# Performance work log

Hardware: AMD Instinct MI355X
Metric: run time of the kernel (lower is better)

## Reference

```python
import jax, jax.numpy as jnp
import numpy as np

ITERS = 3; S = 8; I = 64; E = 64; C = 64; DIN = 128; SLOT = 128; H = 256
B = 64; N = 4096; EPS = 1e-8

def _ln(x, g, b):
    m = jnp.mean(x, -1, keepdims=True)
    v = jnp.var(x, -1, keepdims=True)
    return (x - m) * jax.lax.rsqrt(v + 1e-5) * g + b

def _gru(x, h, Wih, Whh, bih, bhh):
    # torch nn.GRUCell math; W stored as [in, 3*hidden]
    gi = x @ Wih + bih
    gh = h @ Whh + bhh
    ir, iz, inn = jnp.split(gi, 3, -1)
    hr, hz, hn = jnp.split(gh, 3, -1)
    r = jax.nn.sigmoid(ir + hr)
    z = jax.nn.sigmoid(iz + hz)
    n = jnp.tanh(inn + r * hn)
    return (1.0 - z) * n + z * h

def setup_inputs() -> dict:
    k = jax.random.split(jax.random.key(0), 32)
    d = {}
    d['slots_bck'] = jax.random.normal(k[0], (B, 1, SLOT), jnp.float32)
    d['inputs'] = jax.random.normal(k[1], (B, N, DIN), jnp.float32)
    d['protos'] = jax.random.normal(k[2], (C, I), jnp.float32)
    d['ext_noise'] = jax.random.normal(k[3], (B, S, E), jnp.float32)
    d['int_noise'] = jax.random.normal(k[4], (B, S, C), jnp.float32)
    u = jax.random.uniform(k[5], (ITERS, B, S, C), jnp.float32, 1e-6, 1.0 - 1e-6)
    d['gumbel'] = -jnp.log(-jnp.log(u))
    d['tau'] = 1
    w = lambda i, shape, s=0.05: jax.random.normal(k[i], shape, jnp.float32) * s
    d['ext_mu'] = w(6, (1, 1, E)); d['ext_log_sigma'] = w(7, (1, 1, E))
    d['int_mu'] = w(8, (1, 1, C)); d['int_log_sigma'] = w(9, (1, 1, C))
    d['ln_in_g'] = jnp.ones((DIN,)); d['ln_in_b'] = jnp.zeros((DIN,))
    d['ln_p_g'] = jnp.ones((I,)); d['ln_p_b'] = jnp.zeros((I,))
    d['ln_mi_g'] = jnp.ones((I,)); d['ln_mi_b'] = jnp.zeros((I,))
    d['ln_me_g'] = jnp.ones((E,)); d['ln_me_b'] = jnp.zeros((E,))
    d['Wq'] = w(10, (SLOT, SLOT)); d['Wk'] = w(11, (DIN, SLOT))
    d['Wv'] = w(12, (DIN, SLOT)); d['Wp'] = w(13, (I, I))
    d['gi_Wih'] = w(14, (I, 3 * I)); d['gi_Whh'] = w(15, (I, 3 * I))
    d['gi_bih'] = jnp.zeros((3 * I,)); d['gi_bhh'] = jnp.zeros((3 * I,))
    d['ge_Wih'] = w(16, (E, 3 * E)); d['ge_Whh'] = w(17, (E, 3 * E))
    d['ge_bih'] = jnp.zeros((3 * E,)); d['ge_bhh'] = jnp.zeros((3 * E,))
    d['mi_W1'] = w(18, (I, H)); d['mi_b1'] = jnp.zeros((H,))
    d['mi_W2'] = w(19, (H, I)); d['mi_b2'] = jnp.zeros((I,))
    d['me_W1'] = w(20, (E, H)); d['me_b1'] = jnp.zeros((H,))
    d['me_W2'] = w(21, (H, E)); d['me_b2'] = jnp.zeros((E,))
    return d

def reference(slots_bck, inputs, protos, ext_noise, int_noise, gumbel,
              ext_mu, ext_log_sigma, int_mu, int_log_sigma,
              ln_in_g, ln_in_b, ln_p_g, ln_p_b, ln_mi_g, ln_mi_b, ln_me_g, ln_me_b,
              Wq, Wk, Wv, Wp,
              gi_Wih, gi_Whh, gi_bih, gi_bhh, ge_Wih, ge_Whh, ge_bih, ge_bhh,
              mi_W1, mi_b1, mi_W2, mi_b2, me_W1, me_b1, me_W2, me_b2, tau):
    Bsz = inputs.shape[0]
    slots_ext = ext_mu + jnp.exp(ext_log_sigma) * ext_noise            # [B,S,E]
    logits_pi = int_mu + jnp.exp(int_log_sigma) * int_noise            # [B,S,C]
    x = _ln(inputs, ln_in_g, ln_in_b)
    kk = (x @ Wk) * (SLOT ** -0.5)                                     # [B,N,SLOT]
    vv = x @ Wv                                                        # [B,N,SLOT]
    p = _ln(protos, ln_p_g, ln_p_b) @ Wp                               # [C,I]
    attn_vis = None
    for i in range(ITERS):
        pi = jax.nn.softmax((logits_pi + gumbel[i]) / tau, axis=-1)    # soft gumbel-softmax
        slots_int = pi @ p                                             # [B,S,I]
        slots_obj = jnp.concatenate([slots_int, slots_ext], -1)        # [B,S,SLOT]
        slots = jnp.concatenate([slots_bck, slots_obj[:, 1:]], 1)
        q = slots @ Wq                                                 # [B,S,SLOT]
        attn_logits = jnp.einsum('bnd,bsd->bns', kk, q)
        attn_vis = jax.nn.softmax(attn_logits, -1)                     # softmax over slots
        attn = attn_vis + EPS
        attn = attn / jnp.sum(attn, -2, keepdims=True)                 # renorm over inputs
        updates = jnp.einsum('bns,bnd->bsd', attn, vv)                 # [B,S,SLOT]
        upd_int, upd_ext = updates[..., :I], updates[..., I:]
        slots_ext = _gru(upd_ext.reshape(-1, E), slots_ext.reshape(-1, E),
                         ge_Wih, ge_Whh, ge_bih, ge_bhh).reshape(Bsz, S, E)
        if i < ITERS - 1:
            h = _ln(slots_ext, ln_me_g, ln_me_b)
            slots_ext = slots_ext + (jax.nn.relu(h @ me_W1 + me_b1) @ me_W2 + me_b2)
        int_upd = _gru(upd_int.reshape(-1, I), slots_int.reshape(-1, I),
                       gi_Wih, gi_Whh, gi_bih, gi_bhh).reshape(Bsz, S, I)
        if i < ITERS - 1:
            h = _ln(int_upd, ln_mi_g, ln_mi_b)
            int_upd = int_upd + (jax.nn.relu(h @ mi_W1 + mi_b1) @ mi_W2 + mi_b2)
        logits_pi = (int_upd @ p.T) * (I ** -0.5)
    return slots_ext[:, 1:], logits_pi[:, 1:], attn_vis
```

## Files before the change

kernel.cpp:

```cpp
#include <hip/hip_runtime.h>
#include <hip/hip_bf16.h>
#include <stdint.h>

typedef unsigned short u16;
#define DEVFN static __device__ __forceinline__

typedef __attribute__((ext_vector_type(8))) short bf16x8;
typedef __attribute__((ext_vector_type(4))) float f32x4;

constexpr int   kB   = 64;
constexpr int   kN   = 4096;
constexpr float kEPS = 1e-8f;
constexpr float kLNE = 1e-5f;
constexpr float kKSC = 0.08838834764831845f;
constexpr float kISC = 0.125f;

DEVFN u16 f2bf(float f) {
    union { float f; uint32_t u; } x; x.f = f;
    uint32_t r = (x.u + 0x7fffu + ((x.u >> 16) & 1u)) >> 16;
    return (u16)r;
}
DEVFN uint32_t pk2(float lo, float hi) {
    __hip_bfloat162 h = __float22bfloat162_rn(make_float2(lo, hi));
    uint32_t u; __builtin_memcpy(&u, &h, 4); return u;
}
DEVFN u16 bf1(float f) {
    __hip_bfloat16 h = __float2bfloat16(f);
    u16 u; __builtin_memcpy(&u, &h, 2); return u;
}
DEVFN float sigf(float x) { return 1.0f / (1.0f + __expf(-x)); }

__global__ void kinit(const float* __restrict__ ext_mu, const float* __restrict__ ext_ls,
                      const float* __restrict__ int_mu, const float* __restrict__ int_ls,
                      const float* __restrict__ ext_noise, const float* __restrict__ int_noise,
                      float* __restrict__ sext, float* __restrict__ lpi)
{
    int t = blockIdx.x * 256 + threadIdx.x;
    int e = t & 63;
    sext[t] = ext_mu[e] + __expf(ext_ls[e]) * ext_noise[t];
    lpi[t]  = int_mu[e] + __expf(int_ls[e]) * int_noise[t];
}

__global__ void kwprep(const float* __restrict__ Wk, const float* __restrict__ Wv,
                       u16* __restrict__ WT)
{
    int idx = blockIdx.x * 256 + threadIdx.x;
    int k = idx >> 8, c = idx & 255;
    float v = (c < 128) ? Wk[k * 128 + c] * kKSC : Wv[k * 128 + (c - 128)];
    WT[(size_t)c * 128 + k] = f2bf(v);
}

__global__ void kprep(const float* __restrict__ protos, const float* __restrict__ Wp,
                      const float* __restrict__ lpg, const float* __restrict__ lpb,
                      float* __restrict__ p, float* __restrict__ pT)
{
    __shared__ float pl[64][65];
    __shared__ float mS[64], sS[64];
    int t = threadIdx.x;
    for (int idx = t; idx < 64 * 64; idx += 256) pl[idx >> 6][idx & 63] = protos[idx];
    __syncthreads();
    if (t < 64) {
        float sm = 0.f, sq = 0.f;
        for (int k = 0; k < 64; ++k) { float v = pl[t][k]; sm += v; sq += v * v; }
        float m = sm * (1.0f / 64.0f);
        float var = sq * (1.0f / 64.0f) - m * m;
        mS[t] = m; sS[t] = rsqrtf(var + kLNE);
    }
    __syncthreads();
    for (int idx = t; idx < 64 * 64; idx += 256) {
        int r = idx >> 6, c = idx & 63;
        pl[r][c] = (pl[r][c] - mS[r]) * sS[r] * lpg[c] + lpb[c];
    }
    __syncthreads();
    for (int idx = t; idx < 64 * 64; idx += 256) {
        int r = idx >> 6, c = idx & 63;
        float acc = 0.f;
        for (int k = 0; k < 64; ++k) acc += pl[r][k] * Wp[k * 64 + c];
        p[r * 64 + c] = acc;
        pT[c * 64 + r] = acc;
    }
}

__global__ __launch_bounds__(256) void kmain(const float* __restrict__ inputs,
                                             const u16* __restrict__ WT,
                                             const float* __restrict__ lng, const float* __restrict__ lnb,
                                             u16* __restrict__ kk, u16* __restrict__ vvT,
                                             float* __restrict__ vpart)
{
    __shared__ u16 At[64 * 128];
    const int t = threadIdx.x;
    const int blk = blockIdx.x;
    const int b = blk >> 6;
    const int n0 = (blk & 63) * 64;
    const float* inp = inputs + ((size_t)(b * kN + n0)) * 128;

    const int row = t >> 2, q4 = t & 3;
    float4 xv[8];
    #pragma unroll
    for (int j = 0; j < 8; ++j) xv[j] = ((const float4*)inp)[row * 32 + q4 * 8 + j];

    float sm = 0.f, sq = 0.f;
    #pragma unroll
    for (int j = 0; j < 8; ++j) {
        sm += xv[j].x + xv[j].y + xv[j].z + xv[j].w;
        sq += xv[j].x * xv[j].x + xv[j].y * xv[j].y + xv[j].z * xv[j].z + xv[j].w * xv[j].w;
    }
    sm += __shfl_xor(sm, 1); sm += __shfl_xor(sm, 2);
    sq += __shfl_xor(sq, 1); sq += __shfl_xor(sq, 2);
    const float mn  = sm * (1.0f / 128.0f);
    const float var = sq * (1.0f / 128.0f) - mn * mn;
    const float sc  = rsqrtf(var + kLNE);

    const float4* g4p = ((const float4*)lng) + q4 * 8;
    const float4* b4p = ((const float4*)lnb) + q4 * 8;
    #pragma unroll
    for (int jj = 0; jj < 4; ++jj) {
        const float4 a0 = xv[jj * 2], a1 = xv[jj * 2 + 1];
        const float4 g0 = g4p[jj * 2], g1 = g4p[jj * 2 + 1];
        const float4 c0 = b4p[jj * 2], c1 = b4p[jj * 2 + 1];
        uint4 pk;
        pk.x = pk2((a0.x - mn) * sc * g0.x + c0.x, (a0.y - mn) * sc * g0.y + c0.y);
        pk.y = pk2((a0.z - mn) * sc * g0.z + c0.z, (a0.w - mn) * sc * g0.w + c0.w);
        pk.z = pk2((a1.x - mn) * sc * g1.x + c1.x, (a1.y - mn) * sc * g1.y + c1.y);
        pk.w = pk2((a1.z - mn) * sc * g1.z + c1.z, (a1.w - mn) * sc * g1.w + c1.w);
        const int chunk = (q4 * 4 + jj) ^ (row & 7);
        *(uint4*)((char*)At + row * 256 + chunk * 16) = pk;
    }
    __syncthreads();

    const int w  = t >> 6;
    const int l  = t & 63;
    const int lg = l >> 4;
    const int lr = l & 15;
    const bool iskk = (w < 2);

    f32x4 acc[4][4];
    #pragma unroll
    for (int i = 0; i < 4; ++i)
        #pragma unroll
        for (int j = 0; j < 4; ++j) acc[i][j] = (f32x4){0.f, 0.f, 0.f, 0.f};

    #pragma unroll
    for (int ks = 0; ks < 4; ++ks) {
        bf16x8 wf[4], xf[4];
        #pragma unroll
        for (int i = 0; i < 4; ++i)
            wf[i] = *(const bf16x8*)(WT + (size_t)(w * 64 + 16 * i + lr) * 128 + ks * 32 + lg * 8);
        #pragma unroll
        for (int i = 0; i < 4; ++i) {
            const int r2 = 16 * i + lr;
            const int chunk = (ks * 4 + lg) ^ (r2 & 7);
            xf[i] = *(const bf16x8*)((const char*)At + r2 * 256 + chunk * 16);
        }
        if (iskk) {
            #pragma unroll
            for (int i = 0; i < 4; ++i)
                #pragma unroll
                for (int j = 0; j < 4; ++j)
                    acc[i][j] = __builtin_amdgcn_mfma_f32_16x16x32_bf16(wf[i], xf[j], acc[i][j], 0, 0, 0);
        } else {
            #pragma unroll
            for (int i = 0; i < 4; ++i)
                #pragma unroll
                for (int j = 0; j < 4; ++j)
                    acc[i][j] = __builtin_amdgcn_mfma_f32_16x16x32_bf16(xf[i], wf[j], acc[i][j], 0, 0, 0);
        }
    }

    if (iskk) {
        #pragma unroll
        for (int nn = 0; nn < 4; ++nn) {
            const size_t rb = ((size_t)(b * kN) + n0 + 16 * nn + lr) * 128;
            #pragma unroll
            for (int cm = 0; cm < 4; ++cm) {
                uint2 pk;
                pk.x = pk2(acc[cm][nn][0], acc[cm][nn][1]);
                pk.y = pk2(acc[cm][nn][2], acc[cm][nn][3]);
                *(uint2*)(kk + rb + w * 64 + 16 * cm + lg * 4) = pk;
            }
        }
    } else {
        #pragma unroll
        for (int ct = 0; ct < 4; ++ct) {
            const int d = (w - 2) * 64 + 16 * ct + lr;
            const size_t db = ((size_t)b * 128 + d) * (size_t)kN;
            #pragma unroll
            for (int m = 0; m < 4; ++m) {
                uint2 pk;
                pk.x = pk2(acc[m][ct][0], acc[m][ct][1]);
                pk.y = pk2(acc[m][ct][2], acc[m][ct][3]);
                *(uint2*)(vvT + db + n0 + 16 * m + lg * 4) = pk;
            }
            float sv = 0.f;
            #pragma unroll
            for (int m = 0; m < 4; ++m)
                #pragma unroll
                for (int r = 0; r < 4; ++r) sv += acc[m][ct][r];
            sv += __shfl_xor(sv, 16);
            sv += __shfl_xor(sv, 32);
            if (lg == 0) vpart[(size_t)blk * 128 + d] = sv;
        }
    }
}

__global__ void kvvsum(const float* __restrict__ part, float* __restrict__ vvsum)
{
    int t = blockIdx.x * 256 + threadIdx.x;
    int b = t >> 7, c = t & 127;
    float s = 0.f;
    const float* pp = part + (size_t)b * 64 * 128 + c;
    for (int nb = 0; nb < 64; ++nb) s += pp[nb * 128];
    vvsum[t] = s;
}

__global__ void kslots(const float* __restrict__ lpi, const float* __restrict__ gum,
                       const void* __restrict__ taup,
                       const float* __restrict__ p,
                       const float* __restrict__ sbck, const float* __restrict__ sext,
                       const float* __restrict__ Wq,
                       float* __restrict__ sint, float* __restrict__ q)
{
    __shared__ float piL[64];
    __shared__ float sv[128];
    const int bs = blockIdx.x;
    const int b = bs >> 3, s = bs & 7;
    const int t = threadIdx.x;
    float inv_tau = 1.0f;
    {
        int iv = *(const int*)taup;
        if (iv > 0 && iv < 1000000) inv_tau = 1.0f / (float)iv;
        else {
            float fv = *(const float*)taup;
            if (fv > 1e-6f && fv < 1e6f) inv_tau = 1.0f / fv;
        }
    }
    if (t < 64) {
        float l = (lpi[bs * 64 + t] + gum[bs * 64 + t]) * inv_tau;
        float m = l;
        #pragma unroll
        for (int d = 32; d >= 1; d >>= 1) m = fmaxf(m, __shfl_xor(m, d));
        float e = __expf(l - m);
        float smv = e;
        #pragma unroll
        for (int d = 32; d >= 1; d >>= 1) smv += __shfl_xor(smv, d);
        piL[t] = e / smv;
    }
    __syncthreads();
    if (t < 64) {
        float acc = 0.f;
        for (int c = 0; c < 64; ++c) acc += piL[c] * p[c * 64 + t];
        sint[bs * 64 + t] = acc;
        if (s == 0) {
            sv[t]      = sbck[b * 128 + t];
            sv[64 + t] = sbck[b * 128 + 64 + t];
        } else {
            sv[t]      = acc;
            sv[64 + t] = sext[bs * 64 + t];
        }
    }
    __syncthreads();
    {
        float acc = 0.f;
        for (int k = 0; k < 128; ++k) acc += sv[k] * Wq[k * 128 + t];
        q[bs * 128 + t] = acc;
    }
}

__global__ __launch_bounds__(256) void kattn(const u16* __restrict__ kk, const u16* __restrict__ vvT,
                                             const float* __restrict__ q,
                                             float* __restrict__ attn_out,
                                             float* __restrict__ pu, float* __restrict__ pcs,
                                             const int wvis)
{
    __shared__ u16 qbf[16][128];
    __shared__ u16 aB[4][16][40];
    __shared__ float pwU[4][8][132];
    __shared__ float csL[4][8];
    const int t = threadIdx.x;
    const int blk = blockIdx.x;
    const int b = blk >> 3;
    const int nb = blk & 7;
    const int w = t >> 6, l = t & 63, lg = l >> 4, lr = l & 15;

    {
        float4 v = ((const float4*)(q + (size_t)b * 1024))[t];
        uint2 pk;
        pk.x = pk2(v.x, v.y);
        pk.y = pk2(v.z, v.w);
        *(uint2*)&qbf[t >> 5][(t & 31) * 4] = pk;
        ((uint32_t*)qbf)[512 + t] = 0u;
        ((uint32_t*)qbf)[768 + (t & 255)] = 0u;
    }
    __syncthreads();

    bf16x8 qf[4];
    #pragma unroll
    for (int ks = 0; ks < 4; ++ks) qf[ks] = *(const bf16x8*)&qbf[lr][ks * 32 + lg * 8];

    f32x4 apv[8];
    #pragma unroll
    for (int dt = 0; dt < 8; ++dt) apv[dt] = (f32x4){0.f, 0.f, 0.f, 0.f};
    float cs0 = 0.f, cs1 = 0.f, cs2 = 0.f, cs3 = 0.f;

    const size_t kkb = (size_t)(b * kN) * 128;
    const size_t vvb = (size_t)b * 128 * (size_t)kN;

    for (int ch = 0; ch < 4; ++ch) {
        const int nbase = nb * 512 + w * 128 + ch * 32;
        #pragma unroll
        for (int c2 = 0; c2 < 2; ++c2) {
            const int n16 = nbase + 16 * c2;
            f32x4 pl = (f32x4){0.f, 0.f, 0.f, 0.f};
            #pragma unroll
            for (int ks = 0; ks < 4; ++ks) {
                bf16x8 bfr = *(const bf16x8*)(kk + kkb + (size_t)(n16 + lr) * 128 + ks * 32 + lg * 8);
                pl = __builtin_amdgcn_mfma_f32_16x16x32_bf16(qf[ks], bfr, pl, 0, 0, 0);
            }
            float m = fmaxf(fmaxf(pl[0], pl[1]), fmaxf(pl[2], pl[3]));
            m = fmaxf(m, __shfl_xor(m, 16));
            float e0 = __expf(pl[0] - m), e1 = __expf(pl[1] - m);
            float e2 = __expf(pl[2] - m), e3 = __expf(pl[3] - m);
            float smv = e0 + e1 + e2 + e3;
            smv += __shfl_xor(smv, 16);
            const float inv = 1.0f / smv;
            const float a0 = e0 * inv, a1 = e1 * inv, a2 = e2 * inv, a3 = e3 * inv;
            if (lg < 2) {
                cs0 += a0; cs1 += a1; cs2 += a2; cs3 += a3;
                if (wvis)
                    *(float4*)(attn_out + ((size_t)(b * kN) + n16 + lr) * 8 + lg * 4) =
                        make_float4(a0, a1, a2, a3);
                const int s0 = lg * 4, nn = 16 * c2 + lr;
                aB[w][s0 + 0][nn] = bf1(a0);
                aB[w][s0 + 1][nn] = bf1(a1);
                aB[w][s0 + 2][nn] = bf1(a2);
                aB[w][s0 + 3][nn] = bf1(a3);
            }
        }
        bf16x8 af = *(const bf16x8*)&aB[w][lr][lg * 8];
        #pragma unroll
        for (int dt = 0; dt < 8; ++dt) {
            bf16x8 vfr = *(const bf16x8*)(vvT + vvb + (size_t)(16 * dt + lr) * kN + nbase + lg * 8);
            apv[dt] = __builtin_amdgcn_mfma_f32_16x16x32_bf16(vfr, af, apv[dt], 0, 0, 0);
        }
    }

    if (lr < 8) {
        #pragma unroll
        for (int dt = 0; dt < 8; ++dt)
            *(float4*)&pwU[w][lr][16 * dt + lg * 4] =
                make_float4(apv[dt][0], apv[dt][1], apv[dt][2], apv[dt][3]);
    }
    #pragma unroll
    for (int d = 8; d >= 1; d >>= 1) {
        cs0 += __shfl_xor(cs0, d); cs1 += __shfl_xor(cs1, d);
        cs2 += __shfl_xor(cs2, d); cs3 += __shfl_xor(cs3, d);
    }
    if (lr == 0 && lg < 2) {
        csL[w][lg * 4 + 0] = cs0; csL[w][lg * 4 + 1] = cs1;
        csL[w][lg * 4 + 2] = cs2; csL[w][lg * 4 + 3] = cs3;
    }
    __syncthreads();
    {
        const int s = t >> 5, dq = t & 31;
        float4 r0 = *(const float4*)&pwU[0][s][dq * 4];
        float4 r1 = *(const float4*)&pwU[1][s][dq * 4];
        float4 r2 = *(const float4*)&pwU[2][s][dq * 4];
        float4 r3 = *(const float4*)&pwU[3][s][dq * 4];
        float4 o;
        o.x = r0.x + r1.x + r2.x + r3.x;
        o.y = r0.y + r1.y + r2.y + r3.y;
        o.z = r0.z + r1.z + r2.z + r3.z;
        o.w = r0.w + r1.w + r2.w + r3.w;
        *(float4*)(pu + (size_t)blk * 1024 + s * 128 + dq * 4) = o;
    }
    if (t < 8) pcs[blk * 8 + t] = csL[0][t] + csL[1][t] + csL[2][t] + csL[3][t];
}

__global__ __launch_bounds__(256) void kupdate(
    const float* __restrict__ pu, const float* __restrict__ pcs,
    const float* __restrict__ vvsum, const float* __restrict__ sint,
    float* __restrict__ sext, float* __restrict__ lpi,
    const float* __restrict__ giWih, const float* __restrict__ giWhh,
    const float* __restrict__ gibih, const float* __restrict__ gibhh,
    const float* __restrict__ geWih, const float* __restrict__ geWhh,
    const float* __restrict__ gebih, const float* __restrict__ gebhh,
    const float* __restrict__ miW1, const float* __restrict__ mib1,
    const float* __restrict__ miW2, const float* __restrict__ mib2,
    const float* __restrict__ meW1, const float* __restrict__ meb1,
    const float* __restrict__ meW2, const float* __restrict__ meb2,
    const float* __restrict__ lmig, const float* __restrict__ lmib,
    const float* __restrict__ lmeg, const float* __restrict__ lmeb,
    const float* __restrict__ pT, float* __restrict__ out, const int last)
{
    __shared__ float uL[128], hA[64], hB[64];
    __shared__ float g1[192], g2[192];
    __shared__ float tmp[256];
    __shared__ float outE[64], outI[64];
    const int bs = blockIdx.x;
    const int b = bs >> 3, s = bs & 7;
    const int t = threadIdx.x;

    if (t < 128) {
        float num = 0.f;
        for (int nb = 0; nb < 8; ++nb) num += pu[((size_t)(b * 8 + nb)) * 1024 + s * 128 + t];
        float den = 4096.0f * kEPS;
        for (int nb = 0; nb < 8; ++nb) den += pcs[(b * 8 + nb) * 8 + s];
        uL[t] = (num + kEPS * vvsum[b * 128 + t]) / den;
    } else if (t < 192) {
        hA[t - 128] = sext[bs * 64 + (t - 128)];
    } else {
        hB[t - 192] = sint[bs * 64 + (t - 192)];
    }
    __syncthreads();
    if (t < 192) {
        float a = gebih[t], bb = gebhh[t];
        for (int k = 0; k < 64; ++k) {
            a  = fmaf(uL[64 + k], geWih[k * 192 + t], a);
            bb = fmaf(hA[k],      geWhh[k * 192 + t], bb);
        }
        g1[t] = a; g2[t] = bb;
    }
    __syncthreads();
    if (t < 64) {
        float r = sigf(g1[t] + g2[t]);
        float z = sigf(g1[64 + t] + g2[64 + t]);
        float nn = tanhf(g1[128 + t] + r * g2[128 + t]);
        outE[t] = (1.0f - z) * nn + z * hA[t];
    }
    __syncthreads();
    if (t < 192) {
        float a = gibih[t], bb = gibhh[t];
        for (int k = 0; k < 64; ++k) {
            a  = fmaf(uL[k], giWih[k * 192 + t], a);
            bb = fmaf(hB[k], giWhh[k * 192 + t], bb);
        }
        g1[t] = a; g2[t] = bb;
    }
    __syncthreads();
    if (t < 64) {
        float r = sigf(g1[t] + g2[t]);
        float z = sigf(g1[64 + t] + g2[64 + t]);
        float nn = tanhf(g1[128 + t] + r * g2[128 + t]);
        outI[t] = (1.0f - z) * nn + z * hB[t];
    }
    __syncthreads();
    if (!last) {
        if (t < 64) {
            float v = outE[t];
            float sm = v, sq = v * v;
            #pragma unroll
            for (int d = 32; d >= 1; d >>= 1) { sm += __shfl_xor(sm, d); sq += __shfl_xor(sq, d); }
            float m = sm * (1.0f / 64.0f), var = sq * (1.0f / 64.0f) - m * m;
            g1[t] = (v - m) * rsqrtf(var + kLNE) * lmeg[t] + lmeb[t];
        }
        __syncthreads();
        {
            float a = meb1[t];
            for (int k = 0; k < 64; ++k) a = fmaf(g1[k], meW1[k * 256 + t], a);
            tmp[t] = fmaxf(a, 0.0f);
        }
        __syncthreads();
        if (t < 64) {
            float o = meb2[t];
            for (int j = 0; j < 256; ++j) o = fmaf(tmp[j], meW2[j * 64 + t], o);
            outE[t] += o;
        }
        __syncthreads();
        if (t < 64) {
            float v = outI[t];
            float sm = v, sq = v * v;
            #pragma unroll
            for (int d = 32; d >= 1; d >>= 1) { sm += __shfl_xor(sm, d); sq += __shfl_xor(sq, d); }
            float m = sm * (1.0f / 64.0f), var = sq * (1.0f / 64.0f) - m * m;
            g1[t] = (v - m) * rsqrtf(var + kLNE) * lmig[t] + lmib[t];
        }
        __syncthreads();
        {
            float a = mib1[t];
            for (int k = 0; k < 64; ++k) a = fmaf(g1[k], miW1[k * 256 + t], a);
            tmp[t] = fmaxf(a, 0.0f);
        }
        __syncthreads();
        if (t < 64) {
            float o = mib2[t];
            for (int j = 0; j < 256; ++j) o = fmaf(tmp[j], miW2[j * 64 + t], o);
            outI[t] += o;
        }
        __syncthreads();
    }
    if (t < 64) {
        float lg = 0.f;
        for (int k = 0; k < 64; ++k) lg = fmaf(outI[k], pT[k * 64 + t], lg);
        lg *= kISC;
        lpi[bs * 64 + t] = lg;
        if (last && s > 0) out[28672 + (b * 7 + (s - 1)) * 64 + t] = lg;
    } else if (t < 128) {
        int c = t - 64;
        float v = outE[c];
        sext[bs * 64 + c] = v;
        if (last && s > 0) out[(b * 7 + (s - 1)) * 64 + c] = v;
    }
}

extern "C" void kernel_launch(void* const* d_in, const int* in_sizes, int n_in,
                              void* d_out, int out_size, void* d_ws, size_t ws_size,
                              hipStream_t stream)
{
    (void)in_sizes; (void)n_in; (void)out_size; (void)ws_size;
    const float* slots_bck = (const float*)d_in[0];
    const float* inputs    = (const float*)d_in[1];
    const float* protos    = (const float*)d_in[2];
    const float* ext_noise = (const float*)d_in[3];
    const float* int_noise = (const float*)d_in[4];
    const float* gumbel    = (const float*)d_in[5];
    const void*  taup      = d_in[6];
    const float* ext_mu    = (const float*)d_in[7];
    const float* ext_ls    = (const float*)d_in[8];
    const float* int_mu    = (const float*)d_in[9];
    const float* int_ls    = (const float*)d_in[10];
    const float* ln_in_g   = (const float*)d_in[11];
    const float* ln_in_b   = (const float*)d_in[12];
    const float* ln_p_g    = (const float*)d_in[13];
    const float* ln_p_b    = (const float*)d_in[14];
    const float* ln_mi_g   = (const float*)d_in[15];
    const float* ln_mi_b   = (const float*)d_in[16];
    const float* ln_me_g   = (const float*)d_in[17];
    const float* ln_me_b   = (const float*)d_in[18];
    const float* Wq        = (const float*)d_in[19];
    const float* Wk        = (const float*)d_in[20];
    const float* Wv        = (const float*)d_in[21];
    const float* Wp        = (const float*)d_in[22];
    const float* giWih     = (const float*)d_in[23];
    const float* giWhh     = (const float*)d_in[24];
    const float* gibih     = (const float*)d_in[25];
    const float* gibhh     = (const float*)d_in[26];
    const float* geWih     = (const float*)d_in[27];
    const float* geWhh     = (const float*)d_in[28];
    const float* gebih     = (const float*)d_in[29];
    const float* gebhh     = (const float*)d_in[30];
    const float* miW1      = (const float*)d_in[31];
    const float* mib1      = (const float*)d_in[32];
    const float* miW2      = (const float*)d_in[33];
    const float* mib2      = (const float*)d_in[34];
    const float* meW1      = (const float*)d_in[35];
    const float* meb1      = (const float*)d_in[36];
    const float* meW2      = (const float*)d_in[37];
    const float* meb2      = (const float*)d_in[38];
    float* out = (float*)d_out;

    char* ws = (char*)d_ws;
    size_t o = 0;
    auto alloc = [&](size_t bytes) { size_t r = o; o += (bytes + 255) & ~(size_t)255; return r; };
    u16*   kkp   = (u16*)  (ws + alloc((size_t)kB * kN * 128 * 2));
    u16*   vvTp  = (u16*)  (ws + alloc((size_t)kB * kN * 128 * 2));
    u16*   WT    = (u16*)  (ws + alloc(256 * 128 * 2));
    float* vpart = (float*)(ws + alloc((size_t)4096 * 128 * 4));
    float* vvsum = (float*)(ws + alloc(8192 * 4));
    float* pbuf  = (float*)(ws + alloc(4096 * 4));
    float* pT    = (float*)(ws + alloc(4096 * 4));
    float* sext  = (float*)(ws + alloc(32768 * 4));
    float* lpi   = (float*)(ws + alloc(32768 * 4));
    float* sint  = (float*)(ws + alloc(32768 * 4));
    float* q     = (float*)(ws + alloc(65536 * 4));
    float* pu    = (float*)(ws + alloc((size_t)512 * 1024 * 4));
    float* pcs   = (float*)(ws + alloc(512 * 8 * 4));

    kinit<<<128, 256, 0, stream>>>(ext_mu, ext_ls, int_mu, int_ls, ext_noise, int_noise, sext, lpi);
    kwprep<<<128, 256, 0, stream>>>(Wk, Wv, WT);
    kprep<<<1, 256, 0, stream>>>(protos, Wp, ln_p_g, ln_p_b, pbuf, pT);
    kmain<<<4096, 256, 0, stream>>>(inputs, WT, ln_in_g, ln_in_b, kkp, vvTp, vpart);
    kvvsum<<<32, 256, 0, stream>>>(vpart, vvsum);

    for (int i = 0; i < 3; ++i) {
        kslots<<<512, 128, 0, stream>>>(lpi, gumbel + (size_t)i * 32768, taup, pbuf,
                                        slots_bck, sext, Wq, sint, q);
        kattn<<<512, 256, 0, stream>>>(kkp, vvTp, q, out + 57344, pu, pcs, (i == 2) ? 1 : 0);
        kupdate<<<512, 256, 0, stream>>>(pu, pcs, vvsum, sint, sext, lpi,
                                         giWih, giWhh, gibih, gibhh,
                                         geWih, geWhh, gebih, gebhh,
                                         miW1, mib1, miW2, mib2,
                                         meW1, meb1, meW2, meb2,
                                         ln_mi_g, ln_mi_b, ln_me_g, ln_me_b,
                                         pT, out, (i == 2) ? 1 : 0);
    }
}
```

Before: 318.0 us.

## Fuse setup kernels, fold slot/query computation into update kernel, coalesce LN loads

Merges the init, weight-transpose and prototype prep kernels into one launch, folds the vv-sum reduction into the first slots launch, and moves the per-iteration slot sampling and query projection into the tail of the update kernel, so the loop runs two launches per iteration instead of three. The input layernorm in the main kernel now loads with a fully coalesced float4 pattern and reduces across 32 lanes with shuffles. The aim is to cut launch overhead and improve load coalescing. The cost is more shuffle work per row and a longer update kernel.

```diff
diff --git a/kernel.cpp b/kernel.cpp
--- a/kernel.cpp
+++ b/kernel.cpp
@@ -29,34 +29,45 @@
     u16 u; __builtin_memcpy(&u, &h, 2); return u;
 }
 DEVFN float sigf(float x) { return 1.0f / (1.0f + __expf(-x)); }
-
-__global__ void kinit(const float* __restrict__ ext_mu, const float* __restrict__ ext_ls,
-                      const float* __restrict__ int_mu, const float* __restrict__ int_ls,
-                      const float* __restrict__ ext_noise, const float* __restrict__ int_noise,
-                      float* __restrict__ sext, float* __restrict__ lpi)
-{
-    int t = blockIdx.x * 256 + threadIdx.x;
-    int e = t & 63;
-    sext[t] = ext_mu[e] + __expf(ext_ls[e]) * ext_noise[t];
-    lpi[t]  = int_mu[e] + __expf(int_ls[e]) * int_noise[t];
-}
-
-__global__ void kwprep(const float* __restrict__ Wk, const float* __restrict__ Wv,
-                       u16* __restrict__ WT)
-{
-    int idx = blockIdx.x * 256 + threadIdx.x;
-    int k = idx >> 8, c = idx & 255;
-    float v = (c < 128) ? Wk[k * 128 + c] * kKSC : Wv[k * 128 + (c - 128)];
-    WT[(size_t)c * 128 + k] = f2bf(v);
-}
-
-__global__ void kprep(const float* __restrict__ protos, const float* __restrict__ Wp,
-                      const float* __restrict__ lpg, const float* __restrict__ lpb,
-                      float* __restrict__ p, float* __restrict__ pT)
+DEVFN float read_tau(const void* taup) {
+    float inv_tau = 1.0f;
+    int iv = *(const int*)taup;
+    if (iv > 0 && iv < 1000000) inv_tau = 1.0f / (float)iv;
+    else {
+        float fv = *(const float*)taup;
+        if (fv > 1e-6f && fv < 1e6f) inv_tau = 1.0f / fv;
+    }
+    return inv_tau;
+}
+
+__global__ void ksetup(const float* __restrict__ ext_mu, const float* __restrict__ ext_ls,
+                       const float* __restrict__ int_mu, const float* __restrict__ int_ls,
+                       const float* __restrict__ ext_noise, const float* __restrict__ int_noise,
+                       float* __restrict__ sext, float* __restrict__ lpi,
+                       const float* __restrict__ Wk, const float* __restrict__ Wv,
+                       u16* __restrict__ WT,
+                       const float* __restrict__ protos, const float* __restrict__ Wp,
+                       const float* __restrict__ lpg, const float* __restrict__ lpb,
+                       float* __restrict__ p, float* __restrict__ pT)
 {
     __shared__ float pl[64][65];
     __shared__ float mS[64], sS[64];
-    int t = threadIdx.x;
+    const int blk = blockIdx.x;
+    const int t = threadIdx.x;
+    if (blk < 128) {
+        int idx = blk * 256 + t;
+        int e = idx & 63;
+        sext[idx] = ext_mu[e] + __expf(ext_ls[e]) * ext_noise[idx];
+        lpi[idx]  = int_mu[e] + __expf(int_ls[e]) * int_noise[idx];
+        return;
+    }
+    if (blk < 256) {
+        int idx = (blk - 128) * 256 + t;
+        int k = idx >> 8, c = idx & 255;
+        float v = (c < 128) ? Wk[k * 128 + c] * kKSC : Wv[k * 128 + (c - 128)];
+        WT[(size_t)c * 128 + k] = f2bf(v);
+        return;
+    }
     for (int idx = t; idx < 64 * 64; idx += 256) pl[idx >> 6][idx & 63] = protos[idx];
     __syncthreads();
     if (t < 64) {
@@ -94,37 +105,37 @@
     const int n0 = (blk & 63) * 64;
     const float* inp = inputs + ((size_t)(b * kN + n0)) * 128;
 
-    const int row = t >> 2, q4 = t & 3;
     float4 xv[8];
     #pragma unroll
-    for (int j = 0; j < 8; ++j) xv[j] = ((const float4*)inp)[row * 32 + q4 * 8 + j];
-
-    float sm = 0.f, sq = 0.f;
+    for (int j = 0; j < 8; ++j) xv[j] = ((const float4*)inp)[t + j * 256];
+
+    float s[8], qq[8];
     #pragma unroll
     for (int j = 0; j < 8; ++j) {
-        sm += xv[j].x + xv[j].y + xv[j].z + xv[j].w;
-        sq += xv[j].x * xv[j].x + xv[j].y * xv[j].y + xv[j].z * xv[j].z + xv[j].w * xv[j].w;
-    }
-    sm += __shfl_xor(sm, 1); sm += __shfl_xor(sm, 2);
-    sq += __shfl_xor(sq, 1); sq += __shfl_xor(sq, 2);
-    const float mn  = sm * (1.0f / 128.0f);
-    const float var = sq * (1.0f / 128.0f) - mn * mn;
-    const float sc  = rsqrtf(var + kLNE);
-
-    const float4* g4p = ((const float4*)lng) + q4 * 8;
-    const float4* b4p = ((const float4*)lnb) + q4 * 8;
-    #pragma unroll
-    for (int jj = 0; jj < 4; ++jj) {
-        const float4 a0 = xv[jj * 2], a1 = xv[jj * 2 + 1];
-        const float4 g0 = g4p[jj * 2], g1 = g4p[jj * 2 + 1];
-        const float4 c0 = b4p[jj * 2], c1 = b4p[jj * 2 + 1];
-        uint4 pk;
-        pk.x = pk2((a0.x - mn) * sc * g0.x + c0.x, (a0.y - mn) * sc * g0.y + c0.y);
-        pk.y = pk2((a0.z - mn) * sc * g0.z + c0.z, (a0.w - mn) * sc * g0.w + c0.w);
-        pk.z = pk2((a1.x - mn) * sc * g1.x + c1.x, (a1.y - mn) * sc * g1.y + c1.y);
-        pk.w = pk2((a1.z - mn) * sc * g1.z + c1.z, (a1.w - mn) * sc * g1.w + c1.w);
-        const int chunk = (q4 * 4 + jj) ^ (row & 7);
-        *(uint4*)((char*)At + row * 256 + chunk * 16) = pk;
+        s[j]  = xv[j].x + xv[j].y + xv[j].z + xv[j].w;
+        qq[j] = xv[j].x * xv[j].x + xv[j].y * xv[j].y + xv[j].z * xv[j].z + xv[j].w * xv[j].w;
+    }
+    #pragma unroll
+    for (int d = 16; d >= 1; d >>= 1) {
+        #pragma unroll
+        for (int j = 0; j < 8; ++j) {
+            s[j]  += __shfl_xor(s[j], d);
+            qq[j] += __shfl_xor(qq[j], d);
+        }
+    }
+    const int col4 = t & 31;
+    const float4 g4 = ((const float4*)lng)[col4];
+    const float4 b4 = ((const float4*)lnb)[col4];
+    #pragma unroll
+    for (int j = 0; j < 8; ++j) {
+        const int row = (t >> 5) + 8 * j;
+        const float m   = s[j] * (1.0f / 128.0f);
+        const float var = qq[j] * (1.0f / 128.0f) - m * m;
+        const float sc  = rsqrtf(var + kLNE);
+        uint32_t p0 = pk2((xv[j].x - m) * sc * g4.x + b4.x, (xv[j].y - m) * sc * g4.y + b4.y);
+        uint32_t p1 = pk2((xv[j].z - m) * sc * g4.z + b4.z, (xv[j].w - m) * sc * g4.w + b4.w);
+        const int byteoff = row * 256 + (((col4 >> 1) ^ (row & 7)) << 4) + ((col4 & 1) << 3);
+        *(uint2*)((char*)At + byteoff) = make_uint2(p0, p1);
     }
     __syncthreads();
 
@@ -203,37 +214,29 @@
     }
 }
 
-__global__ void kvvsum(const float* __restrict__ part, float* __restrict__ vvsum)
-{
-    int t = blockIdx.x * 256 + threadIdx.x;
-    int b = t >> 7, c = t & 127;
-    float s = 0.f;
-    const float* pp = part + (size_t)b * 64 * 128 + c;
-    for (int nb = 0; nb < 64; ++nb) s += pp[nb * 128];
-    vvsum[t] = s;
-}
-
 __global__ void kslots(const float* __restrict__ lpi, const float* __restrict__ gum,
                        const void* __restrict__ taup,
                        const float* __restrict__ p,
                        const float* __restrict__ sbck, const float* __restrict__ sext,
                        const float* __restrict__ Wq,
-                       float* __restrict__ sint, float* __restrict__ q)
+                       float* __restrict__ sint, float* __restrict__ q,
+                       const float* __restrict__ vpart, float* __restrict__ vvsum)
 {
     __shared__ float piL[64];
     __shared__ float sv[128];
     const int bs = blockIdx.x;
+    const int t = threadIdx.x;
+    if (bs >= 512) {
+        int idx = (bs - 512) * 128 + t;
+        int b = idx >> 7, c = idx & 127;
+        float s = 0.f;
+        const float* pp = vpart + (size_t)b * 64 * 128 + c;
+        for (int nb = 0; nb < 64; ++nb) s += pp[nb * 128];
+        vvsum[idx] = s;
+        return;
+    }
     const int b = bs >> 3, s = bs & 7;
-    const int t = threadIdx.x;
-    float inv_tau = 1.0f;
-    {
-        int iv = *(const int*)taup;
-        if (iv > 0 && iv < 1000000) inv_tau = 1.0f / (float)iv;
-        else {
-            float fv = *(const float*)taup;
-            if (fv > 1e-6f && fv < 1e6f) inv_tau = 1.0f / fv;
-        }
-    }
+    const float inv_tau = read_tau(taup);
     if (t < 64) {
         float l = (lpi[bs * 64 + t] + gum[bs * 64 + t]) * inv_tau;
         float m = l;
@@ -378,7 +381,7 @@
 
 __global__ __launch_bounds__(256) void kupdate(
     const float* __restrict__ pu, const float* __restrict__ pcs,
-    const float* __restrict__ vvsum, const float* __restrict__ sint,
+    const float* __restrict__ vvsum, float* __restrict__ sint,
     float* __restrict__ sext, float* __restrict__ lpi,
     const float* __restrict__ giWih, const float* __restrict__ giWhh,
     const float* __restrict__ gibih, const float* __restrict__ gibhh,
@@ -390,12 +393,17 @@
     const float* __restrict__ meW2, const float* __restrict__ meb2,
     const float* __restrict__ lmig, const float* __restrict__ lmib,
     const float* __restrict__ lmeg, const float* __restrict__ lmeb,
-    const float* __restrict__ pT, float* __restrict__ out, const int last)
+    const float* __restrict__ pT, float* __restrict__ out, const int last,
+    const float* __restrict__ gumN, const void* __restrict__ taup,
+    const float* __restrict__ p, const float* __restrict__ sbck,
+    const float* __restrict__ Wq, float* __restrict__ q)
 {
     __shared__ float uL[128], hA[64], hB[64];
     __shared__ float g1[192], g2[192];
     __shared__ float tmp[256];
     __shared__ float outE[64], outI[64];
+    __shared__ float lgL[64];
+    __shared__ float sv[128];
     const int bs = blockIdx.x;
     const int b = bs >> 3, s = bs & 7;
     const int t = threadIdx.x;
@@ -492,13 +500,47 @@
         float lg = 0.f;
         for (int k = 0; k < 64; ++k) lg = fmaf(outI[k], pT[k * 64 + t], lg);
         lg *= kISC;
-        lpi[bs * 64 + t] = lg;
-        if (last && s > 0) out[28672 + (b * 7 + (s - 1)) * 64 + t] = lg;
+        lgL[t] = lg;
+        if (last) { if (s > 0) out[28672 + (b * 7 + (s - 1)) * 64 + t] = lg; }
     } else if (t < 128) {
         int c = t - 64;
         float v = outE[c];
         sext[bs * 64 + c] = v;
         if (last && s > 0) out[(b * 7 + (s - 1)) * 64 + c] = v;
+    }
+    if (last) return;
+
+    __syncthreads();
+    const float inv_tau = read_tau(taup);
+    if (t < 64) {
+        float l = (lgL[t] + gumN[bs * 64 + t]) * inv_tau;
+        float m = l;
+        #pragma unroll
+        for (int d = 32; d >= 1; d >>= 1) m = fmaxf(m, __shfl_xor(m, d));
+        float e = __expf(l - m);
+        float smv = e;
+        #pragma unroll
+        for (int d = 32; d >= 1; d >>= 1) smv += __shfl_xor(smv, d);
+        tmp[t] = e / smv;
+    }
+    __syncthreads();
+    if (t < 64) {
+        float acc = 0.f;
+        for (int c = 0; c < 64; ++c) acc += tmp[c] * p[c * 64 + t];
+        sint[bs * 64 + t] = acc;
+        if (s == 0) {
+            sv[t]      = sbck[b * 128 + t];
+            sv[64 + t] = sbck[b * 128 + 64 + t];
+        } else {
+            sv[t]      = acc;
+            sv[64 + t] = outE[t];
+        }
+    }
+    __syncthreads();
+    if (t < 128) {
+        float acc = 0.f;
+        for (int k = 0; k < 128; ++k) acc += sv[k] * Wq[k * 128 + t];
+        q[bs * 128 + t] = acc;
     }
 }
 
@@ -565,22 +607,23 @@
     float* pu    = (float*)(ws + alloc((size_t)512 * 1024 * 4));
     float* pcs   = (float*)(ws + alloc(512 * 8 * 4));
 
-    kinit<<<128, 256, 0, stream>>>(ext_mu, ext_ls, int_mu, int_ls, ext_noise, int_noise, sext, lpi);
-    kwprep<<<128, 256, 0, stream>>>(Wk, Wv, WT);
-    kprep<<<1, 256, 0, stream>>>(protos, Wp, ln_p_g, ln_p_b, pbuf, pT);
+    ksetup<<<257, 256, 0, stream>>>(ext_mu, ext_ls, int_mu, int_ls, ext_noise, int_noise,
+                                    sext, lpi, Wk, Wv, WT, protos, Wp, ln_p_g, ln_p_b, pbuf, pT);
     kmain<<<4096, 256, 0, stream>>>(inputs, WT, ln_in_g, ln_in_b, kkp, vvTp, vpart);
-    kvvsum<<<32, 256, 0, stream>>>(vpart, vvsum);
+    kslots<<<576, 128, 0, stream>>>(lpi, gumbel, taup, pbuf, slots_bck, sext, Wq, sint, q,
+                                    vpart, vvsum);
 
     for (int i = 0; i < 3; ++i) {
-        kslots<<<512, 128, 0, stream>>>(lpi, gumbel + (size_t)i * 32768, taup, pbuf,
-                                        slots_bck, sext, Wq, sint, q);
-        kattn<<<512, 256, 0, stream>>>(kkp, vvTp, q, out + 57344, pu, pcs, (i == 2) ? 1 : 0);
+        const int last = (i == 2);
+        kattn<<<512, 256, 0, stream>>>(kkp, vvTp, q, out + 57344, pu, pcs, last ? 1 : 0);
         kupdate<<<512, 256, 0, stream>>>(pu, pcs, vvsum, sint, sext, lpi,
                                          giWih, giWhh, gibih, gibhh,
                                          geWih, geWhh, gebih, gebhh,
                                          miW1, mib1, miW2, mib2,
                                          meW1, meb1, meW2, meb2,
                                          ln_mi_g, ln_mi_b, ln_me_g, ln_me_b,
-                                         pT, out, (i == 2) ? 1 : 0);
-    }
-}
+                                         pT, out, last,
+                                         gumbel + (size_t)(i + 1 < 3 ? i + 1 : 0) * 32768,
+                                         taup, pbuf, slots_bck, Wq, q);
+    }
+}
```

Result: faster. 281.3 us (-11.5%).
